# Kernel tuning notes

Measured on AMD Instinct MI355X. Metric: run time of the kernel, lower is better.

## Reference

```python
import jax, jax.numpy as jnp
import numpy as np

B, T, ENC, DEC, OUT = 4096, 128, 128, 128, 1


def setup_inputs() -> dict:
    key = jax.random.key(0)
    ks = jax.random.split(key, 10)
    def s(k, shape, scale):
        return jax.random.normal(k, shape, jnp.float32) * scale
    return {
        "input_encoded": jax.random.normal(ks[0], (B, T, ENC), jnp.float32),
        "y_history": jax.random.normal(ks[1], (B, T - 1, OUT), jnp.float32),
        # attn_layer: Linear(2*DEC+ENC -> ENC), Tanh, Linear(ENC -> 1)
        "attn_W1": s(ks[2], (ENC, 2 * DEC + ENC), 0.05),
        "attn_b1": jnp.zeros((ENC,), jnp.float32),
        "attn_W2": s(ks[3], (1, ENC), 0.05),
        "attn_b2": jnp.zeros((1,), jnp.float32),
        # LSTM(input_size=OUT, hidden_size=DEC), gate order i,f,g,o
        "W_ih": s(ks[4], (4 * DEC, OUT), 0.08),
        "W_hh": s(ks[5], (4 * DEC, DEC), 0.08),
        "b_ih": jnp.zeros((4 * DEC,), jnp.float32),
        "b_hh": jnp.zeros((4 * DEC,), jnp.float32),
        # fc: Linear(ENC+OUT -> OUT), weight initialized with normal_() (std 1)
        "fc_W": s(ks[6], (OUT, ENC + OUT), 1.0),
        "fc_b": jnp.zeros((OUT,), jnp.float32),
        # fc_final: Linear(DEC+ENC -> OUT)
        "fc_final_W": s(ks[7], (OUT, DEC + ENC), 0.05),
        "fc_final_b": jnp.zeros((OUT,), jnp.float32),
    }


def reference(input_encoded, y_history, attn_W1, attn_b1, attn_W2, attn_b2,
              W_ih, W_hh, b_ih, b_hh, fc_W, fc_b, fc_final_W, fc_final_b):
    Bn, Tn, enc = input_encoded.shape
    dec = W_hh.shape[1]
    # Split attn first-layer weight into hidden / cell / encoded blocks so the
    # concat is never materialized; the encoder projection is loop-invariant.
    W1_h = attn_W1[:, :dec]
    W1_c = attn_W1[:, dec:2 * dec]
    W1_e = attn_W1[:, 2 * dec:]
    enc_proj = jnp.einsum('bte,he->bth', input_encoded, W1_e)  # [B,T,ENC]
    w2 = attn_W2[0]  # [ENC]

    def step(carry, y_t):
        h, c, _ = carry  # h,c: [B,DEC]
        hc_proj = h @ W1_h.T + c @ W1_c.T + attn_b1          # [B,ENC]
        e = jnp.tanh(enc_proj + hc_proj[:, None, :]) @ w2 + attn_b2[0]  # [B,T]
        beta = jax.nn.softmax(e, axis=1)
        context = jnp.einsum('bt,bte->be', beta, input_encoded)  # [B,ENC]
        y_tilde = jnp.concatenate([context, y_t], axis=1) @ fc_W.T + fc_b  # [B,OUT]
        gates = y_tilde @ W_ih.T + b_ih + h @ W_hh.T + b_hh    # [B,4*DEC]
        i, f, g, o = jnp.split(gates, 4, axis=1)
        c_new = jax.nn.sigmoid(f) * c + jax.nn.sigmoid(i) * jnp.tanh(g)
        h_new = jax.nn.sigmoid(o) * jnp.tanh(c_new)
        return (h_new, c_new, context), None

    h0 = jnp.zeros((Bn, dec), jnp.float32)
    c0 = jnp.zeros((Bn, dec), jnp.float32)
    ctx0 = jnp.zeros((Bn, enc), jnp.float32)
    (h, c, context), _ = jax.lax.scan(step, (h0, c0, ctx0),
                                      jnp.swapaxes(y_history, 0, 1))
    return jnp.concatenate([h, context], axis=1) @ fc_final_W.T + fc_final_b
```

## Files before the change

### kernel.cpp

```cpp
#include <hip/hip_runtime.h>
#include <stdint.h>

#define Bsz   4096
#define STEPS 127
#define NTH   512
#define NB    2

typedef float    f4v __attribute__((ext_vector_type(4)));
typedef uint32_t u4v __attribute__((ext_vector_type(4)));
typedef _Float16 h2v __attribute__((ext_vector_type(2)));
typedef __fp16   g2v __attribute__((ext_vector_type(2)));

#define K2E  1.4426950408889634f
#define K2E2 2.8853900817779268f

__device__ __forceinline__ float rcp_f(float x) { return __builtin_amdgcn_rcpf(x); }
__device__ __forceinline__ float exp2_f(float x) {
#if __has_builtin(__builtin_amdgcn_exp2f)
    return __builtin_amdgcn_exp2f(x);
#else
    return exp2f(x);
#endif
}
__device__ __forceinline__ float sig_f(float x)  { return rcp_f(1.f + exp2_f(-K2E * x)); }
__device__ __forceinline__ float tanh_f(float x) { return 1.f - 2.f * rcp_f(1.f + exp2_f(K2E2 * x)); }
__device__ __forceinline__ uint32_t pkh2(float a, float b) {
    union { uint32_t u; g2v h; } v;
    v.h = __builtin_amdgcn_cvt_pkrtz(a, b);
    return v.u;
}
__device__ __forceinline__ float h2lo(uint32_t p) {
    union { uint32_t u; h2v h; } v; v.u = p; return (float)v.h[0];
}
__device__ __forceinline__ float h2hi(uint32_t p) {
    union { uint32_t u; h2v h; } v; v.u = p; return (float)v.h[1];
}
__device__ __forceinline__ float dot2(uint32_t a, uint32_t b, float c) {
    union { uint32_t u; h2v h; } x, y;
    x.u = a; y.u = b;
#if __has_builtin(__builtin_amdgcn_fdot2)
    return __builtin_amdgcn_fdot2(x.h, y.h, c, false);
#else
    return c + (float)x.h[0] * (float)y.h[0] + (float)x.h[1] * (float)y.h[1];
#endif
}

template<int CTRL, int RM, int BM>
__device__ __forceinline__ float dpp_add(float v) {
    union { float f; int i; } s, t;
    s.f = v;
    t.i = __builtin_amdgcn_update_dpp(0, s.i, CTRL, RM, BM, true);
    return v + t.f;
}
template<int CTRL>
__device__ __forceinline__ float dpp_mov(float v) {
    union { float f; int i; } s, t;
    s.f = v;
    t.i = __builtin_amdgcn_mov_dpp(s.i, CTRL, 0xf, 0xf, true);
    return t.f;
}
__device__ __forceinline__ float rd63(float v) {
    union { float f; int i; } s; s.f = v;
    union { int i; float f; } r; r.i = __builtin_amdgcn_readlane(s.i, 63);
    return r.f;
}
__device__ __forceinline__ float qsum(float v) {
    v = dpp_add<0xB1, 0xf, 0xf>(v);
    v = dpp_add<0x4E, 0xf, 0xf>(v);
    return v;
}
__device__ __forceinline__ float wsum(float v) {
    v = dpp_add<0x111, 0xf, 0xf>(v);
    v = dpp_add<0x112, 0xf, 0xf>(v);
    v = dpp_add<0x114, 0xf, 0xe>(v);
    v = dpp_add<0x118, 0xf, 0xc>(v);
    v = dpp_add<0x142, 0xa, 0xf>(v);
    v = dpp_add<0x143, 0xc, 0xf>(v);
    return rd63(v);
}

__global__ __launch_bounds__(NTH, 1)
void dec_kernel(const float* __restrict__ X,
                const float* __restrict__ yh,
                const float* __restrict__ W1,
                const float* __restrict__ b1,
                const float* __restrict__ W2,
                const float* __restrict__ b2u,
                const float* __restrict__ Wih,
                const float* __restrict__ Whh,
                const float* __restrict__ bih,
                const float* __restrict__ bhh,
                const float* __restrict__ fcW,
                const float* __restrict__ fcb,
                const float* __restrict__ Wff,
                const float* __restrict__ bff,
                float* __restrict__ out)
{
    const int tid  = threadIdx.x;
    const int lane = tid & 63;

    __shared__ __align__(16) uint32_t EPT_pk[NB][128 * 68];
    __shared__ __align__(16) float    Xt[8][132];
    __shared__ __align__(16) uint32_t st2[NB][2][144];
    __shared__ __align__(16) float    c32[NB][2][128];
    __shared__ __align__(16) float    h32[NB][128];
    __shared__ __align__(16) float    p_s[NB][128];
    __shared__ __align__(16) float    hc2c[NB][4][36];
    __shared__ __align__(16) float    w2m[4][36];
    __shared__ __align__(16) float    y_s[NB][STEPS + 1];
    __shared__ __align__(16) float    XF[NB][128];
    __shared__ __align__(16) float    XG[NB][128];

    const float* Xb0 = X + (size_t)blockIdx.x * NB * (128 * 128);

    for (int i = tid; i < NB * 2 * 144; i += NTH) ((uint32_t*)st2)[i] = 0u;
    if (tid < 128) { c32[0][0][tid] = 0.f; c32[1][0][tid] = 0.f; }
    if (tid < STEPS) {
        y_s[0][tid] = fcW[128] * yh[(size_t)(blockIdx.x * NB + 0) * STEPS + tid] + fcb[0];
        y_s[1][tid] = fcW[128] * yh[(size_t)(blockIdx.x * NB + 1) * STEPS + tid] + fcb[0];
    }
    if (tid < 128) w2m[tid >> 5][tid & 31] = -2.f * W2[tid];

    const int jA = tid >> 2;
    const int qA = tid & 3;

    #pragma unroll
    for (int bb = 0; bb < NB; ++bb) {
        const float* Xb = Xb0 + bb * (128 * 128);
        float aF = 0.f, aG = 0.f;
        #pragma unroll
        for (int u = 0; u < 8; ++u) {
            f4v xv = *(const f4v*)(Xb + jA * 128 + qA * 32 + 4 * u);
            f4v fv = *(const f4v*)(fcW + qA * 32 + 4 * u);
            f4v gv = *(const f4v*)(Wff + 128 + qA * 32 + 4 * u);
            aF += xv[0]*fv[0] + xv[1]*fv[1] + xv[2]*fv[2] + xv[3]*fv[3];
            aG += xv[0]*gv[0] + xv[1]*gv[1] + xv[2]*gv[2] + xv[3]*gv[3];
        }
        aF = qsum(aF);
        aG = qsum(aG);
        if (qA == 0) { XF[bb][jA] = aF; XG[bb][jA] = aG; }
    }

    {
        float w1e[32];
        #pragma unroll
        for (int u = 0; u < 8; ++u) {
            f4v w = *(const f4v*)(W1 + jA * 384 + 256 + qA * 32 + 4 * u);
            w1e[4*u] = w[0]; w1e[4*u+1] = w[1]; w1e[4*u+2] = w[2]; w1e[4*u+3] = w[3];
        }
        for (int bb = 0; bb < NB; ++bb) {
            const float* Xb = Xb0 + bb * (128 * 128);
            for (int tile = 0; tile < 16; ++tile) {
                __syncthreads();
                if (tid < 256) {
                    int row = tid >> 5, c4 = tid & 31;
                    int p = (c4 & 7) * 4 + (c4 >> 3);
                    *(f4v*)&Xt[row][p * 4] = *(const f4v*)(Xb + (tile * 8 + row) * 128 + c4 * 4);
                }
                __syncthreads();
                #pragma unroll
                for (int tl = 0; tl < 8; ++tl) {
                    float acc = 0.f;
                    #pragma unroll
                    for (int u = 0; u < 8; ++u) {
                        f4v xv = *(const f4v*)&Xt[tl][(u * 4 + qA) * 4];
                        acc += xv[0]*w1e[4*u] + xv[1]*w1e[4*u+1]
                             + xv[2]*w1e[4*u+2] + xv[3]*w1e[4*u+3];
                    }
                    acc = qsum(acc);
                    float accp = __shfl_xor(acc, 4);
                    if ((tid & 7) == 0)
                        EPT_pk[bb][(tile * 8 + tl) * 68 + (tid >> 3)] = pkh2(acc, accp);
                }
            }
        }
    }

    uint32_t w1pk[32];
    #pragma unroll
    for (int m = 0; m < 16; ++m) {
        f4v a = *(const f4v*)(W1 + jA * 384 + qA * 64 + 4 * m);
        w1pk[2*m]   = pkh2(a[0], a[1]);
        w1pk[2*m+1] = pkh2(a[2], a[3]);
    }
    const int jD = tid >> 2;
    const int r  = (tid & 3) * 128 + jD;
    uint32_t whh[64];
    #pragma unroll
    for (int m = 0; m < 32; ++m) {
        f4v w = *(const f4v*)(Whh + (size_t)r * 128 + 4 * m);
        whh[2*m]   = pkh2(w[0], w[1]);
        whh[2*m+1] = pkh2(w[2], w[3]);
    }
    const float wihv = Wih[r];
    const float bgv  = bih[r] + bhh[r];
    const float b1s  = K2E2 * b1[jA];
    float ytg0 = 0.f, ytg1 = 0.f;
    __syncthreads();

    auto PH_A = [&](int b, int s) {
        const int cur = s & 1;
        float a0 = 0.f, a1 = 0.f;
        const uint32_t* sb = &st2[b][cur][qA * 36];
        #pragma unroll
        for (int u = 0; u < 8; ++u) {
            u4v sv = *(const u4v*)(sb + 4 * u);
            a0 = dot2(sv[0], w1pk[4*u],   a0);
            a1 = dot2(sv[1], w1pk[4*u+1], a1);
            a0 = dot2(sv[2], w1pk[4*u+2], a0);
            a1 = dot2(sv[3], w1pk[4*u+3], a1);
        }
        float acc = qsum(a0 + a1);
        if (qA == 0) hc2c[b][jA >> 5][jA & 31] = fmaf(K2E2, acc, b1s);
    };

    auto PH_B = [&](int b) {
        const int tt = tid >> 2, q = tid & 3;
        const uint32_t* er = &EPT_pk[b][tt * 68 + q * 16];
        u4v ee0 = *(const u4v*)(er);
        u4v ee1 = *(const u4v*)(er + 4);
        u4v ee2 = *(const u4v*)(er + 8);
        u4v ee3 = *(const u4v*)(er + 12);
        float acc = 0.f;
        #pragma unroll
        for (int u = 0; u < 4; ++u) {
            u4v ev = (u == 0) ? ee0 : (u == 1) ? ee1 : (u == 2) ? ee2 : ee3;
            f4v hcv = *(const f4v*)&hc2c[b][q][8 * u];
            f4v hcw = *(const f4v*)&hc2c[b][q][8 * u + 4];
            f4v wv  = *(const f4v*)&w2m[q][8 * u];
            f4v wvw = *(const f4v*)&w2m[q][8 * u + 4];
            #pragma unroll
            for (int m = 0; m < 4; ++m) {
                uint32_t ep = ev[m];
                float hl = (m < 2) ? hcv[2*m]   : hcw[2*m-4];
                float hh = (m < 2) ? hcv[2*m+1] : hcw[2*m-3];
                float wl = (m < 2) ? wv[2*m]    : wvw[2*m-4];
                float wh = (m < 2) ? wv[2*m+1]  : wvw[2*m-3];
                float z0 = exp2_f(fmaf(h2lo(ep), K2E2, hl));
                float z1 = exp2_f(fmaf(h2hi(ep), K2E2, hh));
                acc = fmaf(wl, rcp_f(1.f + z0), acc);
                acc = fmaf(wh, rcp_f(1.f + z1), acc);
            }
        }
        acc = qsum(acc);
        float pt = exp2_f(K2E * acc);
        if (q == 0) p_s[b][tt] = pt;
    };

    auto PH_C = [&](int b, int s, float& ytg_ref) {
        const int cur = s & 1;
        float d0 = 0.f, d1 = 0.f, d2 = 0.f, d3 = 0.f;
        const uint32_t* hb = &st2[b][cur][0];
        #pragma unroll
        for (int m = 0; m < 8; ++m) {
            u4v sv = *(const u4v*)(hb + 4 * m);
            d0 = dot2(sv[0], whh[4*m],   d0);
            d1 = dot2(sv[1], whh[4*m+1], d1);
            d2 = dot2(sv[2], whh[4*m+2], d2);
            d3 = dot2(sv[3], whh[4*m+3], d3);
        }
        #pragma unroll
        for (int m = 0; m < 8; ++m) {
            u4v sv = *(const u4v*)(hb + 36 + 4 * m);
            d0 = dot2(sv[0], whh[32 + 4*m],   d0);
            d1 = dot2(sv[1], whh[32 + 4*m+1], d1);
            d2 = dot2(sv[2], whh[32 + 4*m+2], d2);
            d3 = dot2(sv[3], whh[32 + 4*m+3], d3);
        }
        float gdot = (d0 + d1) + (d2 + d3);
        float v0 = p_s[b][lane], v1 = p_s[b][lane + 64];
        float sp = wsum(v0 + v1);
        float sf = wsum(v0 * XF[b][lane] + v1 * XF[b][lane + 64]);
        float sg = wsum(v0 * XG[b][lane] + v1 * XG[b][lane + 64]);
        float inv = rcp_f(sp);
        float ytc = sf * inv;
        ytg_ref   = sg * inv;
        float g  = gdot + fmaf(wihv, ytc + y_s[b][s], bgv);
        float gb = dpp_mov<0xB1>(g);
        float gc = dpp_mov<0x4E>(g);
        float gd = dpp_mov<0x4E>(gb);
        if ((tid & 3) == 0) {
            float co = c32[b][cur][jD];
            float cn = sig_f(gb) * co + sig_f(g) * tanh_f(gc);
            float hn = sig_f(gd) * tanh_f(cn);
            c32[b][cur ^ 1][jD] = cn;
            h32[b][jD] = hn;
            float hp = __shfl_xor(hn, 4);
            float cp = __shfl_xor(cn, 4);
            if ((tid & 7) == 0) {
                int m0 = tid >> 3;
                int sl = m0 + 4 * (m0 >> 5);
                st2[b][cur ^ 1][sl]      = pkh2(hn, hp);
                st2[b][cur ^ 1][72 + sl] = pkh2(cn, cp);
            }
        }
    };

    PH_A(0, 0);
    __syncthreads();
    PH_B(0);  PH_A(1, 0);
    __syncthreads();

    for (int s = 0; s < STEPS - 1; ++s) {
        PH_C(0, s, ytg0);      PH_B(1);
        __syncthreads();
        PH_A(0, s + 1);        PH_C(1, s, ytg1);
        __syncthreads();
        PH_B(0);               PH_A(1, s + 1);
        __syncthreads();
    }
    PH_C(0, STEPS - 1, ytg0);  PH_B(1);
    __syncthreads();
    PH_C(1, STEPS - 1, ytg1);
    __syncthreads();

    if (tid < 64) {
        float v0 = h32[0][lane] * Wff[lane] + h32[0][lane + 64] * Wff[lane + 64];
        v0 = wsum(v0);
        float v1 = h32[1][lane] * Wff[lane] + h32[1][lane + 64] * Wff[lane + 64];
        v1 = wsum(v1);
        if (lane == 0) {
            out[blockIdx.x * NB + 0] = v0 + ytg0 + bff[0];
            out[blockIdx.x * NB + 1] = v1 + ytg1 + bff[0];
        }
    }
}

extern "C" void kernel_launch(void* const* d_in, const int* in_sizes, int n_in,
                              void* d_out, int out_size, void* d_ws, size_t ws_size,
                              hipStream_t stream) {
    dec_kernel<<<Bsz / NB, NTH, 0, stream>>>(
        (const float*)d_in[0],  (const float*)d_in[1],  (const float*)d_in[2],
        (const float*)d_in[3],  (const float*)d_in[4],  (const float*)d_in[5],
        (const float*)d_in[6],  (const float*)d_in[7],  (const float*)d_in[8],
        (const float*)d_in[9],  (const float*)d_in[10], (const float*)d_in[11],
        (const float*)d_in[12], (const float*)d_in[13], (float*)d_out);
}
```

Measured before the change: 4.577 ms.

## Split LSTM gate dot from softmax reduction and hoist it earlier in schedule

Splits the recurrent W_hh dot product out of phase C and computes it right after the new h/c state is available, in the phase before the softmax-context reduction. This moves that dot off the critical phase and lets it run alongside other phases. It also interleaves the p_s, XF and XG shared arrays so each lane reads its two values with one 2-wide load instead of two scalar loads. The reordered schedule relies on the state being ready after the barrier and keeps two extra live registers.

```diff
diff --git a/kernel.cpp b/kernel.cpp
--- a/kernel.cpp
+++ b/kernel.cpp
@@ -7,6 +7,7 @@
 #define NB    2
 
 typedef float    f4v __attribute__((ext_vector_type(4)));
+typedef float    f2v __attribute__((ext_vector_type(2)));
 typedef uint32_t u4v __attribute__((ext_vector_type(4)));
 typedef _Float16 h2v __attribute__((ext_vector_type(2)));
 typedef __fp16   g2v __attribute__((ext_vector_type(2)));
@@ -108,8 +109,8 @@
     __shared__ __align__(16) float    hc2c[NB][4][36];
     __shared__ __align__(16) float    w2m[4][36];
     __shared__ __align__(16) float    y_s[NB][STEPS + 1];
-    __shared__ __align__(16) float    XF[NB][128];
-    __shared__ __align__(16) float    XG[NB][128];
+    __shared__ __align__(16) float    XFa[NB][128];
+    __shared__ __align__(16) float    XGa[NB][128];
 
     const float* Xb0 = X + (size_t)blockIdx.x * NB * (128 * 128);
 
@@ -138,7 +139,8 @@
         }
         aF = qsum(aF);
         aG = qsum(aG);
-        if (qA == 0) { XF[bb][jA] = aF; XG[bb][jA] = aG; }
+        int sl = (jA & 63) * 2 + (jA >> 6);
+        if (qA == 0) { XFa[bb][sl] = aF; XGa[bb][sl] = aG; }
     }
 
     {
@@ -244,10 +246,10 @@
         }
         acc = qsum(acc);
         float pt = exp2_f(K2E * acc);
-        if (q == 0) p_s[b][tt] = pt;
+        if (q == 0) p_s[b][(tt & 63) * 2 + (tt >> 6)] = pt;
     };
 
-    auto PH_C = [&](int b, int s, float& ytg_ref) {
+    auto PH_Ddot = [&](int b, int s) -> float {
         const int cur = s & 1;
         float d0 = 0.f, d1 = 0.f, d2 = 0.f, d3 = 0.f;
         const uint32_t* hb = &st2[b][cur][0];
@@ -267,11 +269,17 @@
             d2 = dot2(sv[2], whh[32 + 4*m+2], d2);
             d3 = dot2(sv[3], whh[32 + 4*m+3], d3);
         }
-        float gdot = (d0 + d1) + (d2 + d3);
-        float v0 = p_s[b][lane], v1 = p_s[b][lane + 64];
-        float sp = wsum(v0 + v1);
-        float sf = wsum(v0 * XF[b][lane] + v1 * XF[b][lane + 64]);
-        float sg = wsum(v0 * XG[b][lane] + v1 * XG[b][lane + 64]);
+        return (d0 + d1) + (d2 + d3);
+    };
+
+    auto PH_Cs = [&](int b, int s, float gdot, float& ytg_ref) {
+        const int cur = s & 1;
+        f2v pv = *(const f2v*)&p_s[b][2 * lane];
+        f2v xf = *(const f2v*)&XFa[b][2 * lane];
+        f2v xg = *(const f2v*)&XGa[b][2 * lane];
+        float sp = wsum(pv[0] + pv[1]);
+        float sf = wsum(pv[0] * xf[0] + pv[1] * xf[1]);
+        float sg = wsum(pv[0] * xg[0] + pv[1] * xg[1]);
         float inv = rcp_f(sp);
         float ytc = sf * inv;
         ytg_ref   = sg * inv;
@@ -296,22 +304,28 @@
         }
     };
 
-    PH_A(0, 0);
-    __syncthreads();
-    PH_B(0);  PH_A(1, 0);
+    float gdot0, gdot1;
+    PH_A(0, 0);  gdot0 = PH_Ddot(0, 0);
+    __syncthreads();
+    PH_B(0);  PH_A(1, 0);  gdot1 = PH_Ddot(1, 0);
     __syncthreads();
 
     for (int s = 0; s < STEPS - 1; ++s) {
-        PH_C(0, s, ytg0);      PH_B(1);
+        PH_Cs(0, s, gdot0, ytg0);
+        PH_B(1);
         __syncthreads();
-        PH_A(0, s + 1);        PH_C(1, s, ytg1);
+        PH_A(0, s + 1);
+        gdot0 = PH_Ddot(0, s + 1);
+        PH_Cs(1, s, gdot1, ytg1);
         __syncthreads();
-        PH_B(0);               PH_A(1, s + 1);
+        PH_B(0);
+        PH_A(1, s + 1);
+        gdot1 = PH_Ddot(1, s + 1);
         __syncthreads();
     }
-    PH_C(0, STEPS - 1, ytg0);  PH_B(1);
-    __syncthreads();
-    PH_C(1, STEPS - 1, ytg1);
+    PH_Cs(0, STEPS - 1, gdot0, ytg0);  PH_B(1);
+    __syncthreads();
+    PH_Cs(1, STEPS - 1, gdot1, ytg1);
     __syncthreads();
 
     if (tid < 64) {
```

Measured after the change: 4.686 ms. 2.4% more time.
